# Performance work log

Measured on AMD Instinct MI355X. Metric: run time of the kernel, lower is better.

Reference implementation:

```python
import jax, jax.numpy as jnp
import numpy as np

N = 8_000_000
LOG_HALF = -0.6931471805599453  # log(1/2)

DATASET_MAP = {0: 0, 1: 0, 2: 0, 3: 0, 4: 1, 5: 1, 6: 1, 7: 1}
LOSS_RECIPE = [(0, 4, 4), (0, 6, 4), (1, 5, 5), (1, 6, 5), (2, 4, 4), (2, 5, 5), (2, 6, 6), (2, 7, 7),
               (4, 0, 4), (4, 2, 4), (5, 1, 5), (5, 2, 5), (6, 2, 6), (7, 2, 7)]
NEG_LOSS_RECIPE = [(0, 4, 1), (0, 4, 2), (0, 6, 1), (0, 6, 2), (1, 5, 0), (1, 5, 2), (1, 6, 0), (1, 6, 2),
                   (2, 4, 1), (2, 4, 2), (2, 5, 0), (2, 5, 2), (4, 0, 1), (4, 0, 2), (4, 2, 1), (4, 2, 2),
                   (5, 1, 0), (5, 1, 2), (5, 2, 0), (5, 2, 2), (2, 7, 2), (7, 2, 2)]


def log1mexp(x):
    """Numerically stable log(1 - exp(x)) for x < 0 (grad-safe where)."""
    big = x > LOG_HALF
    xb = jnp.where(big, x, -1.0)   # branch-safe operands
    xs = jnp.where(big, -1.0, x)
    return jnp.where(big, jnp.log(-jnp.expm1(xb)), jnp.log1p(-jnp.exp(xs)))


def create_probabilities(v1, v2):
    l1, l2 = log1mexp(v1), log1mexp(v2)
    return [v1 + l2, l1 + v2, v1 + v2, l1 + l2]  # PC, CP, CR, NR


def setup_inputs() -> dict:
    key = jax.random.key(0)
    ks = jax.random.split(key, 9)
    def vol(k):
        u = jax.random.uniform(k, (N, 2), dtype=jnp.float32, minval=1e-6, maxval=1.0 - 1e-6)
        return jnp.log(u)  # strictly negative log-probabilities
    names = ["vol_AB", "vol_BA", "vol_BC", "vol_CB", "vol_AC", "vol_CA"]
    inp = {n: vol(k) for n, k in zip(names, ks[:6])}
    inp["xy_rel_id"] = jax.random.randint(ks[6], (N, 2), 0, 2)
    inp["yz_rel_id"] = jax.random.randint(ks[7], (N, 2), 0, 2)
    inp["xz_rel_id"] = jax.random.randint(ks[8], (N, 2), 0, 2)
    return inp


def reference(vol_AB, vol_BA, vol_BC, vol_CB, vol_AC, vol_CA, xy_rel_id, yz_rel_id, xz_rel_id):
    pAB = create_probabilities(vol_AB, vol_BA)
    pBC = create_probabilities(vol_BC, vol_CB)
    pAC = create_probabilities(vol_AC, vol_CA)
    loss = jnp.float32(0.0)
    for xy, yz, xz in LOSS_RECIPE:
        f1, f2, f3 = DATASET_MAP[xy], DATASET_MAP[yz], DATASET_MAP[xz]
        term = pAB[xy % 4][:, f1] + pBC[yz % 4][:, f2] - pAC[xz % 4][:, f3]
        loss = loss + jnp.maximum(0.0, term).sum()
    for xy, yz, xz in NEG_LOSS_RECIPE:
        f1, f2, f3 = DATASET_MAP[xy], DATASET_MAP[yz], DATASET_MAP[xz]
        term = pAB[xy % 4][:, f1] + pBC[yz % 4][:, f2] - log1mexp(pAC[xz % 4][:, f3])
        loss = loss + jnp.maximum(0.0, term).sum()
    return loss
```

## Files before the change

kernel.cpp:

```cpp
#include <hip/hip_runtime.h>


#define LOG2E 1.4426950408889634f
#define LN2   0.6931471805599453f

__device__ __forceinline__ float fexp2(float x) { return __builtin_amdgcn_exp2f(x); }
__device__ __forceinline__ float flog2(float x) { return __builtin_amdgcn_logf(x); }
__device__ __forceinline__ float relu_(float x) { return fmaxf(x, 0.0f); }

__device__ __forceinline__ float row_loss_l2(
    float a0, float a1, float b0, float b1,
    float c0, float c1, float d0, float d1,
    float e0, float e1, float f0, float f1)
{
    float a0s = a0 * LOG2E, a1s = a1 * LOG2E;
    float b0s = b0 * LOG2E, b1s = b1 * LOG2E;
    float c0s = c0 * LOG2E, c1s = c1 * LOG2E;
    float d0s = d0 * LOG2E, d1s = d1 * LOG2E;
    float e0s = e0 * LOG2E, e1s = e1 * LOG2E;
    float f0s = f0 * LOG2E, f1s = f1 * LOG2E;

    float ua0 = fexp2(a0s), ub0 = fexp2(b0s), uc0 = fexp2(c0s), ud0 = fexp2(d0s);
    float ue0 = fexp2(e0s), uf0 = fexp2(f0s);
    float ua1 = fexp2(a1s), ub1 = fexp2(b1s), uc1 = fexp2(c1s), ud1 = fexp2(d1s);
    float ue1 = fexp2(e1s), uf1 = fexp2(f1s);

    float wa0 = 1.0f - ua0, wb0 = 1.0f - ub0, wc0 = 1.0f - uc0, wd0 = 1.0f - ud0;
    float we0 = 1.0f - ue0, wf0 = 1.0f - uf0;
    float wa1 = 1.0f - ua1, wb1 = 1.0f - ub1, wc1 = 1.0f - uc1, wd1 = 1.0f - ud1;
    float we1 = 1.0f - ue1, wf1 = 1.0f - uf1;

    float la0 = flog2(wa0), lb0 = flog2(wb0), lc0 = flog2(wc0), ld0 = flog2(wd0);
    float la1 = flog2(wa1), lb1 = flog2(wb1), lc1 = flog2(wc1), ld1 = flog2(wd1);
    float le1 = flog2(we1), lf1 = flog2(wf1);

    float LAC0 = flog2(fmaf(-ue0, wf0, 1.0f));
    float LAC1 = flog2(fmaf(-we0, uf0, 1.0f));
    float LAC2 = flog2(fmaf(-ue0, uf0, 1.0f));

    float AB00 = a0s + lb0, AB10 = la0 + b0s, AB20 = a0s + b0s;
    float AB01 = a1s + lb1, AB11 = la1 + b1s, AB21 = a1s + b1s, AB31 = la1 + lb1;
    float BC00 = c0s + ld0, BC10 = lc0 + d0s, BC20 = c0s + d0s;
    float BC01 = c1s + ld1, BC11 = lc1 + d1s, BC21 = c1s + d1s, BC31 = lc1 + ld1;
    float AC01 = e1s + lf1, AC11 = le1 + f1s, AC21 = e1s + f1s, AC31 = le1 + lf1;

    float s1  = AB00 + BC01, s2  = AB00 + BC21, s3  = AB10 + BC11, s4  = AB10 + BC21;
    float s5  = AB20 + BC01, s6  = AB20 + BC11, s7  = AB20 + BC21, s8  = AB20 + BC31;
    float s9  = AB01 + BC00, s10 = AB01 + BC20, s11 = AB11 + BC10, s12 = AB11 + BC20;
    float s13 = AB21 + BC20, s14 = AB31 + BC20;

    float p = 0.0f, q = 0.0f;
    p += relu_(s1 - AC01) + relu_(s2 - AC01) + relu_(s3 - AC11) + relu_(s4 - AC11);
    q += relu_(s5 - AC01) + relu_(s6 - AC11) + relu_(s7 - AC21) + relu_(s8 - AC31);
    p += relu_(s9 - AC01) + relu_(s10 - AC01) + relu_(s11 - AC11) + relu_(s12 - AC11);
    q += relu_(s13 - AC21) + relu_(s14 - AC31);
    p += relu_(s1 - LAC1) + relu_(s1 - LAC2) + relu_(s2 - LAC1) + relu_(s2 - LAC2);
    q += relu_(s3 - LAC0) + relu_(s3 - LAC2) + relu_(s4 - LAC0) + relu_(s4 - LAC2);
    p += relu_(s5 - LAC1) + relu_(s5 - LAC2) + relu_(s6 - LAC0) + relu_(s6 - LAC2);
    q += relu_(s9 - LAC1) + relu_(s9 - LAC2) + relu_(s10 - LAC1) + relu_(s10 - LAC2);
    p += relu_(s11 - LAC0) + relu_(s11 - LAC2) + relu_(s12 - LAC0) + relu_(s12 - LAC2);
    q += relu_(s8 - LAC2) + relu_(s14 - LAC2);
    return p + q;
}

__device__ __forceinline__ float pair_loss(float4 ab, float4 ba, float4 bc,
                                           float4 cb, float4 ac, float4 ca)
{
    return row_loss_l2(ab.x, ab.y, ba.x, ba.y, bc.x, bc.y,
                       cb.x, cb.y, ac.x, ac.y, ca.x, ca.y)
         + row_loss_l2(ab.z, ab.w, ba.z, ba.w, bc.z, bc.w,
                       cb.z, cb.w, ac.z, ac.w, ca.z, ca.w);
}

__global__ __launch_bounds__(256, 4) void box_loss_kernel(
    const float* __restrict__ AB, const float* __restrict__ BA,
    const float* __restrict__ BC, const float* __restrict__ CB,
    const float* __restrict__ AC, const float* __restrict__ CA,
    float* __restrict__ out, int nElems)
{
    const long chunk = (long)blockIdx.x * 2048;
    const int  t     = threadIdx.x;
    const long b0    = chunk + 4 * t;
    const long b1    = chunk + 1024 + 4 * t;
    const long nE    = (long)nElems;

    const bool v0 = (b0 + 4) <= nE;
    const bool v1 = (b1 + 4) <= nE;
    const long a0 = v0 ? b0 : 0;
    const long a1 = v1 ? b1 : 0;
    const float m0 = v0 ? 1.0f : 0.0f;
    const float m1 = v1 ? 1.0f : 0.0f;

    float4 ab0 = *(const float4*)(AB + a0);
    float4 ba0 = *(const float4*)(BA + a0);
    float4 bc0 = *(const float4*)(BC + a0);
    float4 cb0 = *(const float4*)(CB + a0);
    float4 ac0 = *(const float4*)(AC + a0);
    float4 ca0 = *(const float4*)(CA + a0);
    float4 ab1 = *(const float4*)(AB + a1);
    float4 ba1 = *(const float4*)(BA + a1);
    float4 bc1 = *(const float4*)(BC + a1);
    float4 cb1 = *(const float4*)(CB + a1);
    float4 ac1 = *(const float4*)(AC + a1);
    float4 ca1 = *(const float4*)(CA + a1);

    float acc = m0 * pair_loss(ab0, ba0, bc0, cb0, ac0, ca0)
              + m1 * pair_loss(ab1, ba1, bc1, cb1, ac1, ca1);

    acc *= LN2;

    #pragma unroll
    for (int off = 32; off > 0; off >>= 1)
        acc += __shfl_down(acc, off, 64);

    __shared__ float wsum[4];
    const int lane = threadIdx.x & 63;
    const int wid  = threadIdx.x >> 6;
    if (lane == 0) wsum[wid] = acc;
    __syncthreads();
    if (threadIdx.x == 0) {
        float s = wsum[0] + wsum[1] + wsum[2] + wsum[3];
        atomicAdd(out, s);
    }
}

extern "C" void kernel_launch(void* const* d_in, const int* in_sizes, int n_in,
                              void* d_out, int out_size, void* d_ws, size_t ws_size,
                              hipStream_t stream) {
    const float* AB = (const float*)d_in[0];
    const float* BA = (const float*)d_in[1];
    const float* BC = (const float*)d_in[2];
    const float* CB = (const float*)d_in[3];
    const float* AC = (const float*)d_in[4];
    const float* CA = (const float*)d_in[5];

    const long nElems = in_sizes[0];
    const long nChunks = (nElems + 2047) / 2048;
    const int block = 256;
    const int grid = (int)nChunks;

    hipMemsetAsync(d_out, 0, (size_t)out_size * sizeof(float), stream);
    box_loss_kernel<<<grid, block, 0, stream>>>(AB, BA, BC, CB, AC, CA,
                                                (float*)d_out, (int)nElems);
}
```

Measured before the change: 452.2 us.

## Use persistent grid-stride loop with software-prefetched register double buffering

Replaces the one-chunk-per-block launch with a fixed 2048-block grid in which each thread walks the data with a grid stride. The next segment's six float4 loads are issued before the current segment is computed, and a sched_barrier keeps the compiler from reordering them past that point. The aim is to hide memory latency behind the heavy transcendental math and cut block launch and atomic overhead. In exchange it doubles live registers for the input segments, which can pressure occupancy under launch_bounds(256,4).

Result: faster. 439.7 us (-2.8%).

```diff
diff --git a/kernel.cpp b/kernel.cpp
--- a/kernel.cpp
+++ b/kernel.cpp
@@ -63,49 +63,58 @@
     return p + q;
 }
 
-__device__ __forceinline__ float pair_loss(float4 ab, float4 ba, float4 bc,
-                                           float4 cb, float4 ac, float4 ca)
+struct Seg {
+    float4 ab, ba, bc, cb, ac, ca;
+};
+
+__device__ __forceinline__ float pair_loss(const Seg& s)
 {
-    return row_loss_l2(ab.x, ab.y, ba.x, ba.y, bc.x, bc.y,
-                       cb.x, cb.y, ac.x, ac.y, ca.x, ca.y)
-         + row_loss_l2(ab.z, ab.w, ba.z, ba.w, bc.z, bc.w,
-                       cb.z, cb.w, ac.z, ac.w, ca.z, ca.w);
+    return row_loss_l2(s.ab.x, s.ab.y, s.ba.x, s.ba.y, s.bc.x, s.bc.y,
+                       s.cb.x, s.cb.y, s.ac.x, s.ac.y, s.ca.x, s.ca.y)
+         + row_loss_l2(s.ab.z, s.ab.w, s.ba.z, s.ba.w, s.bc.z, s.bc.w,
+                       s.cb.z, s.cb.w, s.ac.z, s.ac.w, s.ca.z, s.ca.w);
 }
 
 __global__ __launch_bounds__(256, 4) void box_loss_kernel(
     const float* __restrict__ AB, const float* __restrict__ BA,
     const float* __restrict__ BC, const float* __restrict__ CB,
     const float* __restrict__ AC, const float* __restrict__ CA,
-    float* __restrict__ out, int nElems)
+    float* __restrict__ out, long nElems)
 {
-    const long chunk = (long)blockIdx.x * 2048;
-    const int  t     = threadIdx.x;
-    const long b0    = chunk + 4 * t;
-    const long b1    = chunk + 1024 + 4 * t;
-    const long nE    = (long)nElems;
+    const long nE = nElems;
+    const long stride = (long)gridDim.x * blockDim.x * 4;
+    long idx = ((long)blockIdx.x * blockDim.x + threadIdx.x) * 4;
+    const int nIter = (int)((nE + stride - 1) / stride);
 
-    const bool v0 = (b0 + 4) <= nE;
-    const bool v1 = (b1 + 4) <= nE;
-    const long a0 = v0 ? b0 : 0;
-    const long a1 = v1 ? b1 : 0;
-    const float m0 = v0 ? 1.0f : 0.0f;
-    const float m1 = v1 ? 1.0f : 0.0f;
+    #define LOAD_SEG(dst, msk, base)                        \
+        do {                                                \
+            bool v_ = ((base) + 4) <= nE;                   \
+            long a_ = v_ ? (base) : 0;                      \
+            (msk) = v_ ? 1.0f : 0.0f;                       \
+            (dst).ab = *(const float4*)(AB + a_);           \
+            (dst).ba = *(const float4*)(BA + a_);           \
+            (dst).bc = *(const float4*)(BC + a_);           \
+            (dst).cb = *(const float4*)(CB + a_);           \
+            (dst).ac = *(const float4*)(AC + a_);           \
+            (dst).ca = *(const float4*)(CA + a_);           \
+        } while (0)
 
-    float4 ab0 = *(const float4*)(AB + a0);
-    float4 ba0 = *(const float4*)(BA + a0);
-    float4 bc0 = *(const float4*)(BC + a0);
-    float4 cb0 = *(const float4*)(CB + a0);
-    float4 ac0 = *(const float4*)(AC + a0);
-    float4 ca0 = *(const float4*)(CA + a0);
-    float4 ab1 = *(const float4*)(AB + a1);
-    float4 ba1 = *(const float4*)(BA + a1);
-    float4 bc1 = *(const float4*)(BC + a1);
-    float4 cb1 = *(const float4*)(CB + a1);
-    float4 ac1 = *(const float4*)(AC + a1);
-    float4 ca1 = *(const float4*)(CA + a1);
+    float acc = 0.0f;
+    Seg cur, nxt;
+    float mcur, mnxt;
+    LOAD_SEG(cur, mcur, idx);
+    long p = idx + stride;
 
-    float acc = m0 * pair_loss(ab0, ba0, bc0, cb0, ac0, ca0)
-              + m1 * pair_loss(ab1, ba1, bc1, cb1, ac1, ca1);
+    for (int it = 1; it < nIter; ++it) {
+        LOAD_SEG(nxt, mnxt, p);
+        __builtin_amdgcn_sched_barrier(0);
+        acc += mcur * pair_loss(cur);
+        cur = nxt;
+        mcur = mnxt;
+        p += stride;
+    }
+    acc += mcur * pair_loss(cur);
+    #undef LOAD_SEG
 
     acc *= LN2;
 
@@ -135,11 +144,10 @@
     const float* CA = (const float*)d_in[5];
 
     const long nElems = in_sizes[0];
-    const long nChunks = (nElems + 2047) / 2048;
     const int block = 256;
-    const int grid = (int)nChunks;
+    const int grid = 2048;
 
     hipMemsetAsync(d_out, 0, (size_t)out_size * sizeof(float), stream);
     box_loss_kernel<<<grid, block, 0, stream>>>(AB, BA, BC, CB, AC, CA,
-                                                (float*)d_out, (int)nElems);
+                                                (float*)d_out, nElems);
 }
```
